# Performance work log

Measured on AMD Instinct MI355X. Metric: run time of the kernel, lower is better.

Reference implementation:

```python
import jax, jax.numpy as jnp
import numpy as np
from jax.scipy.linalg import expm

# dims: batch B_, seq S_, d_inner Di, d_state Ds (must equal Di), dt_rank R
B_, S_, Di, Ds, R = 16, 512, 64, 64, 4


def setup_inputs() -> dict:
    key = jax.random.key(0)
    k0, k1, k2, k3 = jax.random.split(key, 4)
    x = jax.random.normal(k0, (B_, S_, Di), dtype=jnp.float32)
    # x_proj: Linear(Di -> R + 2*Ds); small init keeps dt small so expm stays finite
    Wx = jax.random.normal(k1, (R + 2 * Ds, Di), dtype=jnp.float32) * 0.05
    bx = jax.random.normal(k2, (R + 2 * Ds,), dtype=jnp.float32) * 0.05
    # dt_proj: Linear(R -> Di)
    Wdt = jax.random.normal(k3, (Di, R), dtype=jnp.float32) * 0.01
    bdt = jnp.zeros((Di,), dtype=jnp.float32)
    # A_log[d, n] = log(n+1), matching repeat(arange(1..Ds), 'n -> d n')
    A_log = jnp.log(jnp.broadcast_to(jnp.arange(1, Ds + 1, dtype=jnp.float32), (Di, Ds)))
    Dp = jnp.ones((Di,), dtype=jnp.float32)
    return {"x": x, "Wx": Wx, "bx": bx, "Wdt": Wdt, "bdt": bdt, "A_log": A_log, "Dp": Dp}


def _ssm_forward(x, Wx, bx, Wdt, bdt, A_log, Dp):
    b = x.shape[0]
    A = -jnp.exp(A_log)                    # (Di, Ds)
    I = jnp.eye(Di, Ds, dtype=x.dtype)     # (Di, Ds), square here
    expm_b = jax.vmap(expm)                # batched matrix exponential

    def step(hs, xi):
        # xi: (b, Di)
        proj = xi @ Wx.T + bx              # (b, R + 2*Ds)
        Bm = proj[:, :Ds]                  # (b, Ds)
        dtr = proj[:, Ds:Ds + R]           # (b, R)
        Cm = proj[:, Ds + R:]              # (b, Ds)
        dt = dtr @ Wdt.T + bdt             # (b, Di)
        deltaA = dt[:, :, None] * A[None]  # (b, Di, Ds) = diag(dt) @ A
        dA = expm_b(deltaA)                # exact discretization: exp(dt*A)
        deltaB = dt[:, :, None] * Bm[:, None, :]           # (b, Di, Ds)
        dB = jnp.linalg.pinv(deltaA) @ (dA - I) @ deltaB   # (dtA)^+ (e^{dtA}-I) dtB
        hs = hs * dA + xi[:, :, None] * dB
        mask = (jnp.abs(xi).sum(-1) > 1e-5).astype(x.dtype)[:, None, None]
        hs = hs * mask + jax.lax.stop_gradient(hs) * (1.0 - mask)
        hs = jnp.clip(hs, -1e6, 1e6)
        y = jnp.einsum('bdn,bn->bd', hs, Cm) + Dp * xi
        return hs, (y, hs)

    hs0 = jnp.zeros((b, Di, Ds), dtype=x.dtype)
    _, (ys, hss) = jax.lax.scan(step, hs0, jnp.swapaxes(x, 0, 1))
    # original returns (y of the LAST timestep, all hidden states (b, seq, Di, Ds))
    return ys[-1], jnp.swapaxes(hss, 0, 1)


def reference(x, Wx, bx, Wdt, bdt, A_log, Dp):
    return _ssm_forward(x, Wx, bx, Wdt, bdt, A_log, Dp)
```

## Files before the change

kernel.cpp:

```cpp
#include <hip/hip_runtime.h>
#include <cmath>

#define B_  16
#define S_  512
#define DI  64
#define DS  64
#define RR  4

typedef float f32x4 __attribute__((ext_vector_type(4)));

#define WS_U    524288
#define WS_BM   1048576
#define WS_CML  1572864

__global__ __launch_bounds__(64)
void ssm_k1(const float* __restrict__ x, const float* __restrict__ Wx,
            const float* __restrict__ bx, const float* __restrict__ Wdt,
            const float* __restrict__ bdt, const float* __restrict__ A_log,
            float* __restrict__ ws)
{
    __shared__ float xs[DI];
    __shared__ float dtr_s[RR];
    const int bt   = blockIdx.x;
    const int lane = threadIdx.x;

    const float xv = x[bt * DI + lane];
    xs[lane] = xv;
    const float a_l = -expf(A_log[lane]);
    __syncthreads();

    float accB = bx[lane];
    {
        const float* wr = Wx + lane * DI;
        #pragma unroll
        for (int i = 0; i < DI; i += 4) {
            f32x4 w = *reinterpret_cast<const f32x4*>(wr + i);
            accB += w.x * xs[i] + w.y * xs[i + 1] + w.z * xs[i + 2] + w.w * xs[i + 3];
        }
    }
    if (lane < RR) {
        float acc = bx[DS + lane];
        const float* wr = Wx + (DS + lane) * DI;
        #pragma unroll
        for (int i = 0; i < DI; i += 4) {
            f32x4 w = *reinterpret_cast<const f32x4*>(wr + i);
            acc += w.x * xs[i] + w.y * xs[i + 1] + w.z * xs[i + 2] + w.w * xs[i + 3];
        }
        dtr_s[lane] = acc;
    }
    __syncthreads();

    float dtv = bdt[lane];
    #pragma unroll
    for (int r = 0; r < RR; ++r) dtv += dtr_s[r] * Wdt[lane * RR + r];

    float sv = a_l * dtv;
    float qv = a_l * a_l;
    #pragma unroll
    for (int off = 32; off > 0; off >>= 1) {
        sv += __shfl_xor(sv, off);
        qv += __shfl_xor(qv, off);
    }

    const float E   = expm1f(sv);
    const float phi = (fabsf(sv) < 1e-3f)
                        ? fmaf(sv, fmaf(sv, 1.0f / 6.0f, 0.5f), 1.0f)
                        : (E / sv);

    ws[bt * DI + lane]          = phi * dtv;
    ws[WS_U + bt * DI + lane]   = xv * (E / qv) * a_l;
    ws[WS_BM + bt * DI + lane]  = accB;

    if ((bt & (S_ - 1)) == (S_ - 1)) {
        float accC = bx[DS + RR + lane];
        const float* wr = Wx + (DS + RR + lane) * DI;
        #pragma unroll
        for (int i = 0; i < DI; i += 4) {
            f32x4 w = *reinterpret_cast<const f32x4*>(wr + i);
            accC += w.x * xs[i] + w.y * xs[i + 1] + w.z * xs[i + 2] + w.w * xs[i + 3];
        }
        ws[WS_CML + (bt >> 9) * DS + lane] = accC;
    }
}

__global__ __launch_bounds__(256)
void ssm_k2(const float* __restrict__ ws, const float* __restrict__ x,
            const float* __restrict__ A_log, const float* __restrict__ Dp,
            float* __restrict__ out)
{
    const int tid  = threadIdx.x;
    const int n    = tid & 63;
    const int dsub = tid >> 6;
    const int b    = blockIdx.x >> 4;
    const int dg   = blockIdx.x & 15;
    const int d    = dg * 4 + dsub;

    const float a_n   = -expf(A_log[n]);
    const float delta = (d == n) ? 1.0f : 0.0f;

    const float* __restrict__ phidt = ws + (size_t)(b * S_) * DI + d;
    const float* __restrict__ uws   = ws + WS_U + (size_t)(b * S_) * DI + d;
    const float* __restrict__ bmws  = ws + WS_BM + (size_t)(b * S_) * DI + n;
    float* __restrict__ po = out + 1024 + (size_t)(b * S_) * (DI * DS) + d * DS + n;

    float h = 0.0f;
    for (int tb = 0; tb < S_; tb += 16) {
        float pv[16], uv[16], bv[16];
        #pragma unroll
        for (int j = 0; j < 16; ++j) {
            pv[j] = phidt[(size_t)(tb + j) * DI];
            uv[j] = uws[(size_t)(tb + j) * DI];
            bv[j] = bmws[(size_t)(tb + j) * DI];
        }
        #pragma unroll
        for (int j = 0; j < 16; ++j) {
            const float av = fmaf(pv[j], a_n, delta);
            h = fmaf(av, h, uv[j] * bv[j]);
            h = fminf(fmaxf(h, -1.0e6f), 1.0e6f);
            po[(size_t)(tb + j) * (DI * DS)] = h;
        }
    }

    const float* cml = ws + WS_CML;
    float v = h * cml[b * DS + n];
    #pragma unroll
    for (int off = 32; off > 0; off >>= 1) v += __shfl_xor(v, off);
    if (n == 0) {
        const float xi = x[((b * S_) + S_ - 1) * DI + d];
        out[b * DI + d] = v + Dp[d] * xi;
    }
}

extern "C" void kernel_launch(void* const* d_in, const int* in_sizes, int n_in,
                              void* d_out, int out_size, void* d_ws, size_t ws_size,
                              hipStream_t stream)
{
    const float* x     = (const float*)d_in[0];
    const float* Wx    = (const float*)d_in[1];
    const float* bx    = (const float*)d_in[2];
    const float* Wdt   = (const float*)d_in[3];
    const float* bdt   = (const float*)d_in[4];
    const float* A_log = (const float*)d_in[5];
    const float* Dp    = (const float*)d_in[6];
    float* out = (float*)d_out;
    float* ws  = (float*)d_ws;

    ssm_k1<<<B_ * S_, 64, 0, stream>>>(x, Wx, bx, Wdt, bdt, A_log, ws);
    ssm_k2<<<B_ * 16, 256, 0, stream>>>(ws, x, A_log, Dp, out);
}
```

Measured before the change: 61.17 us.

## Stage scan inputs through double-buffered LDS with register prefetch in k2

The scan kernel now cooperatively loads 64-timestep chunks of the phi*dt, u and B inputs into shared memory using vectorized loads, double-buffered, with the next chunk prefetched into registers while the current chunk is scanned. This replaces per-thread strided scalar global loads, which were redundant across waves, with coalesced loads and LDS reads. It adds two barriers per chunk and about 33KB of LDS per block. The dominant cost, the large hidden-state output store, is unchanged.

```diff
diff --git a/kernel.cpp b/kernel.cpp
--- a/kernel.cpp
+++ b/kernel.cpp
@@ -6,6 +6,7 @@
 #define DI  64
 #define DS  64
 #define RR  4
+#define CLIPM 1.0e6f
 
 typedef float f32x4 __attribute__((ext_vector_type(4)));
 
@@ -88,37 +89,74 @@
             const float* __restrict__ A_log, const float* __restrict__ Dp,
             float* __restrict__ out)
 {
-    const int tid  = threadIdx.x;
-    const int n    = tid & 63;
-    const int dsub = tid >> 6;
-    const int b    = blockIdx.x >> 4;
-    const int dg   = blockIdx.x & 15;
-    const int d    = dg * 4 + dsub;
+    __shared__ float pd_s[2][64][4];
+    __shared__ float ud_s[2][64][4];
+    __shared__ float bm_s[2][64][64];
+
+    const int tid = threadIdx.x;
+    const int n   = tid & 63;
+    const int wid = tid >> 6;
+    const int b   = blockIdx.x >> 4;
+    const int dg  = blockIdx.x & 15;
+    const int d   = dg * 4 + wid;
 
     const float a_n   = -expf(A_log[n]);
     const float delta = (d == n) ? 1.0f : 0.0f;
 
-    const float* __restrict__ phidt = ws + (size_t)(b * S_) * DI + d;
-    const float* __restrict__ uws   = ws + WS_U + (size_t)(b * S_) * DI + d;
-    const float* __restrict__ bmws  = ws + WS_BM + (size_t)(b * S_) * DI + n;
+    const float* pg = ws + (size_t)(b * S_) * DI;
+    const float* ug = ws + WS_U + (size_t)(b * S_) * DI;
+    const float* bg = ws + WS_BM + (size_t)(b * S_) * DI;
     float* __restrict__ po = out + 1024 + (size_t)(b * S_) * (DI * DS) + d * DS + n;
 
+    const int js = tid >> 2;
+    const int dc = tid & 3;
+
+    f32x4 rb[4]; float rp, ru;
+
+    #pragma unroll
+    for (int p = 0; p < 4; ++p)
+        rb[p] = *reinterpret_cast<const f32x4*>(bg + (size_t)(p * 256 + tid) * 4);
+    rp = pg[(size_t)js * DI + dg * 4 + dc];
+    ru = ug[(size_t)js * DI + dg * 4 + dc];
+    #pragma unroll
+    for (int p = 0; p < 4; ++p)
+        *reinterpret_cast<f32x4*>(&bm_s[0][0][0] + (size_t)(p * 256 + tid) * 4) = rb[p];
+    pd_s[0][js][dc] = rp;
+    ud_s[0][js][dc] = ru;
+    __syncthreads();
+
     float h = 0.0f;
-    for (int tb = 0; tb < S_; tb += 16) {
-        float pv[16], uv[16], bv[16];
-        #pragma unroll
-        for (int j = 0; j < 16; ++j) {
-            pv[j] = phidt[(size_t)(tb + j) * DI];
-            uv[j] = uws[(size_t)(tb + j) * DI];
-            bv[j] = bmws[(size_t)(tb + j) * DI];
+    for (int c = 0; c < 8; ++c) {
+        const int buf = c & 1;
+        const int t0  = c * 64;
+        if (c < 7) {
+            const size_t t1 = (size_t)(t0 + 64);
+            #pragma unroll
+            for (int p = 0; p < 4; ++p)
+                rb[p] = *reinterpret_cast<const f32x4*>(bg + t1 * DS + (size_t)(p * 256 + tid) * 4);
+            rp = pg[(t1 + js) * DI + dg * 4 + dc];
+            ru = ug[(t1 + js) * DI + dg * 4 + dc];
         }
-        #pragma unroll
-        for (int j = 0; j < 16; ++j) {
-            const float av = fmaf(pv[j], a_n, delta);
-            h = fmaf(av, h, uv[j] * bv[j]);
-            h = fminf(fmaxf(h, -1.0e6f), 1.0e6f);
-            po[(size_t)(tb + j) * (DI * DS)] = h;
+        #pragma unroll 8
+        for (int j = 0; j < 64; ++j) {
+            const float pv = pd_s[buf][j][wid];
+            const float uv = ud_s[buf][j][wid];
+            const float bv = bm_s[buf][j][n];
+            const float av = fmaf(pv, a_n, delta);
+            h = fmaf(av, h, uv * bv);
+            h = fminf(fmaxf(h, -CLIPM), CLIPM);
+            po[(size_t)(t0 + j) * (DI * DS)] = h;
         }
+        __syncthreads();
+        if (c < 7) {
+            const int nb = buf ^ 1;
+            #pragma unroll
+            for (int p = 0; p < 4; ++p)
+                *reinterpret_cast<f32x4*>(&bm_s[nb][0][0] + (size_t)(p * 256 + tid) * 4) = rb[p];
+            pd_s[nb][js][dc] = rp;
+            ud_s[nb][js][dc] = ru;
+        }
+        __syncthreads();
     }
 
     const float* cml = ws + WS_CML;
```

After: 60.97 us. About the same (-0.3%).
